# Kernel tuning notes

Measured on AMD Instinct MI355X. Metric: run time of the kernel, lower is better.

The kernel has to match this reference:

```python
import jax, jax.numpy as jnp
import numpy as np

N = 2048       # num nodes
E = 4096       # num edges
D_NODE = 128
D_EDGE = 128
H = 4          # heads
DH = D_EDGE // H
C = 16         # num classes
NODE_K = N // 2   # node_k_ratio = 0.5
EDGE_K = E // 2   # edge_k_ratio = 0.5
NEG = -1e9


def setup_inputs() -> dict:
    key = jax.random.key(0)
    ks = jax.random.split(key, 16)
    w = lambda k, shape: jax.random.normal(k, shape, jnp.float32) * 0.02
    return {
        "node_features": jax.random.normal(ks[0], (N, D_NODE), jnp.float32),
        "edge_features": jax.random.normal(ks[1], (E, D_EDGE), jnp.float32),
        "edge_index": jax.random.randint(ks[2], (2, E), 0, N, jnp.int32),
        # ImportanceRouter: scalar scores per node / edge
        "w_router_n": w(ks[3], (D_NODE,)),
        "w_router_e": w(ks[4], (D_EDGE,)),
        # EdgeAttention projections
        "w_e": w(ks[5], (D_EDGE, D_EDGE)),
        "w_n": w(ks[6], (D_NODE, D_EDGE)),
        "w_q": w(ks[7], (D_EDGE, D_EDGE)),
        "w_k": w(ks[8], (D_EDGE, D_EDGE)),
        "w_v": w(ks[9], (D_EDGE, D_EDGE)),
        "w_o": w(ks[10], (D_EDGE, D_EDGE)),
        # classifier MLP: Linear -> GELU -> Linear
        "w1": w(ks[11], (D_EDGE, D_EDGE)),
        "b1": jnp.zeros((D_EDGE,), jnp.float32),
        "w2": w(ks[12], (D_EDGE, C)),
        "b2": jnp.zeros((C,), jnp.float32),
    }


def reference(node_features, edge_features, edge_index,
              w_router_n, w_router_e,
              w_e, w_n, w_q, w_k, w_v, w_o,
              w1, b1, w2, b2):
    src, dst = edge_index[0], edge_index[1]

    # --- ImportanceRouter: node/edge scores ---
    ns = node_features @ w_router_n   # [N]
    es = edge_features @ w_router_e   # [E]

    # --- apply_top_k(node_k_ratio=0.5, edge_k_ratio=0.5) ---
    _, nidx = jax.lax.top_k(ns, NODE_K)
    node_mask = jnp.zeros((N,), bool).at[nidx].set(True)
    _, eidx = jax.lax.top_k(es, EDGE_K)
    edge_topk = jnp.zeros((E,), bool).at[eidx].set(True)
    edge_mask = edge_topk & node_mask[src] & node_mask[dst]   # [E]

    ef = edge_features * edge_mask[:, None].astype(edge_features.dtype)

    # --- build_edge_adjacency: edges sharing a node attend to each other ---
    adj = ((src[:, None] == src[None, :]) | (src[:, None] == dst[None, :]) |
           (dst[:, None] == src[None, :]) | (dst[:, None] == dst[None, :]))  # [E,E]

    # --- EdgeAttention: edge rep mixes edge feats and endpoint node feats ---
    h = ef @ w_e + (node_features[src] + node_features[dst]) @ w_n   # [E, D_EDGE]
    q = (h @ w_q).reshape(E, H, DH)
    k = (h @ w_k).reshape(E, H, DH)
    v = (h @ w_v).reshape(E, H, DH)
    scores = jnp.einsum('ehd,fhd->hef', q, k) / np.float32(np.sqrt(DH))  # [H,E,E]
    scores = jnp.where(adj[None, :, :], scores, NEG)
    attn = jax.nn.softmax(scores, axis=-1)
    o = jnp.einsum('hef,fhd->ehd', attn, v).reshape(E, D_EDGE) @ w_o    # [E, D_EDGE]

    # --- classifier: Linear -> GELU -> Linear ---
    x = jax.nn.gelu(o @ w1 + b1)
    logits = x @ w2 + b2            # [E, C]
    return logits
```

## Files before the change

### kernel.cpp

```cpp
#include <hip/hip_runtime.h>
#include <hip/hip_bf16.h>
#include <math.h>

#define NN 2048
#define NE 4096
#define D 128
#define NODE_K 1024
#define EDGE_K 2048
#define CAP 64

typedef const __hip_bfloat16* bfp;
typedef unsigned short u16;
typedef __attribute__((ext_vector_type(8))) short short8;
typedef __attribute__((ext_vector_type(4))) float floatx4;

#define MFMA16(a, b, c) __builtin_amdgcn_mfma_f32_16x16x32_bf16(a, b, c, 0, 0, 0)

__device__ __forceinline__ float b2f(__hip_bfloat16 x) { return __bfloat162float(x); }

__device__ __forceinline__ float ldx(const void* p, size_t i, int f) {
  return f ? ((const float*)p)[i] : b2f(((bfp)p)[i]);
}

__device__ __forceinline__ void split2(float x, u16& hi, u16& lo) {
  unsigned u = __float_as_uint(x);
  unsigned h = (u + 0x7FFFu + ((u >> 16) & 1u)) >> 16;
  hi = (u16)h;
  float r = x - __uint_as_float(h << 16);
  unsigned v = __float_as_uint(r);
  lo = (u16)((v + 0x7FFFu + ((v >> 16) & 1u)) >> 16);
}
__device__ __forceinline__ void build_frags(const float* v8, short8& fh, short8& fl) {
  #pragma unroll
  for (int i = 0; i < 8; ++i) {
    u16 h, l;
    split2(v8[i], h, l);
    fh[i] = (short)h; fl[i] = (short)l;
  }
}

__device__ __forceinline__ int detect_f(const u16* raw, int* s4) {
  int t = threadIdx.x;
  int weird = 0;
  for (int i = t; i < 4096; i += blockDim.x) {
    unsigned int bits = ((unsigned int)raw[i]) << 16;
    float x = __uint_as_float(bits);
    float ax = fabsf(x);
    if (!(ax <= 1e3f) || (x != 0.f && ax < 1e-12f)) weird++;
  }
  #pragma unroll
  for (int m = 32; m >= 1; m >>= 1) weird += __shfl_xor(weird, m);
  int nw = (int)blockDim.x >> 6;
  if ((t & 63) == 0) s4[t >> 6] = weird;
  __syncthreads();
  int tot = 0;
  for (int i = 0; i < nw; ++i) tot += s4[i];
  return (tot > 200) ? 1 : 0;
}

struct K1Args {
  const void *nf, *ef, *wrn, *wre;
  const void* w[7];
  float *ns, *es;
  int *deg, *flag;
  u16 *wtHi, *wtLo;
  u16 *feHi, *feLo;
};

#define SCORE_BLOCKS ((NN + NE) / 4)
#define WPREP_BLOCKS 56
#define FSPLIT_BLOCKS 384
__global__ __launch_bounds__(256) void scores_prep_kernel(K1Args a) {
  __shared__ int s4[4];
  int b = blockIdx.x, t = threadIdx.x;
  int f = detect_f((const u16*)a.nf, s4);
  if (b < SCORE_BLOCKS) {
    int wid = b * 4 + (t >> 6), lane = t & 63;
    const void* base; const void* w; float* out; size_t r0;
    if (wid < NN) { base = a.nf; r0 = (size_t)wid * D; w = a.wrn; out = a.ns + wid; }
    else { int r = wid - NN; base = a.ef; r0 = (size_t)r * D; w = a.wre; out = a.es + r; }
    double p = (double)ldx(base, r0 + lane, f) * (double)ldx(w, lane, f)
             + (double)ldx(base, r0 + lane + 64, f) * (double)ldx(w, lane + 64, f);
    #pragma unroll
    for (int m = 32; m >= 1; m >>= 1) p += __shfl_xor(p, m);
    if (lane == 0) *out = (float)p;
  } else if (b == SCORE_BLOCKS) {
    if (t == 0) a.flag[0] = f;
    for (int i = t; i < NN; i += 256) a.deg[i] = 0;
  } else if (b <= SCORE_BLOCKS + WPREP_BLOCKS) {
    int wb = b - SCORE_BLOCKS - 1;
    #pragma unroll
    for (int i = 0; i < 8; ++i) {
      int g = wb * 2048 + i * 256 + t;
      int w = g >> 14, r = g & 16383;
      int k = r >> 7, n = r & 127;
      u16 hi, lo;
      split2(ldx(a.w[w], r, f), hi, lo);
      a.wtHi[w * 16384 + n * 128 + k] = hi;
      a.wtLo[w * 16384 + n * 128 + k] = lo;
    }
  } else {
    int fb = b - SCORE_BLOCKS - 1 - WPREP_BLOCKS;
    #pragma unroll
    for (int i = 0; i < 8; ++i) {
      int g = fb * 2048 + i * 256 + t;
      float x = (g < NN * D) ? ldx(a.nf, g, f) : ldx(a.ef, g - NN * D, f);
      u16 hi, lo;
      split2(x, hi, lo);
      a.feHi[g] = hi; a.feLo[g] = lo;
    }
  }
}

#define NMB (NN / 4)
#define EMB (NE / 4)
__global__ __launch_bounds__(256) void mask_lists_kernel(
    const float* __restrict__ ns, const float* __restrict__ es,
    const int* __restrict__ src, const int* __restrict__ dst,
    int* __restrict__ node_mask, int* __restrict__ edge_topk,
    int* __restrict__ deg, int* __restrict__ lists) {
  __shared__ float s[NE];
  int b = blockIdx.x, t = threadIdx.x;
  if (b < NMB) {
    for (int i = t; i < NN; i += 256) s[i] = ns[i];
    __syncthreads();
    int i = b * 4 + (t >> 6), lane = t & 63;
    float si = s[i];
    int rank = 0;
    for (int j = lane; j < NN; j += 64) {
      float sj = s[j];
      rank += (sj > si) || (sj == si && j < i);
    }
    #pragma unroll
    for (int m = 32; m >= 1; m >>= 1) rank += __shfl_xor(rank, m);
    if (lane == 0) node_mask[i] = (rank < NODE_K) ? 1 : 0;
  } else if (b < NMB + EMB) {
    for (int i = t; i < NE; i += 256) s[i] = es[i];
    __syncthreads();
    int i = (b - NMB) * 4 + (t >> 6), lane = t & 63;
    float si = s[i];
    int rank = 0;
    for (int j = lane; j < NE; j += 64) {
      float sj = s[j];
      rank += (sj > si) || (sj == si && j < i);
    }
    #pragma unroll
    for (int m = 32; m >= 1; m >>= 1) rank += __shfl_xor(rank, m);
    if (lane == 0) edge_topk[i] = (rank < EDGE_K) ? 1 : 0;
  } else {
    int e = (b - NMB - EMB) * 256 + t;
    if (e < NE) {
      int sn = src[e], dn = dst[e];
      int p = atomicAdd(&deg[sn], 1);
      if (p >= 0 && p < CAP) lists[sn * CAP + p] = e;
      if (dn != sn) {
        p = atomicAdd(&deg[dn], 1);
        if (p >= 0 && p < CAP) lists[dn * CAP + p] = e;
      }
    }
  }
}

__global__ __launch_bounds__(512) void h_qkv_mfma_kernel(
    const u16* __restrict__ feHi, const u16* __restrict__ feLo,
    const int* __restrict__ src, const int* __restrict__ dst,
    const int* __restrict__ node_mask, const int* __restrict__ edge_topk,
    const u16* __restrict__ wtHi, const u16* __restrict__ wtLo,
    float* __restrict__ qkv) {
  __shared__ __align__(16) float hf[8 * 64 * 4];
  int t = threadIdx.x;
  int wave = t >> 6, lane = t & 63;
  int qd = lane >> 4, c = lane & 15;
  int row0 = blockIdx.x * 16;
  int e = row0 + c;
  int sn = src[e], dn = dst[e];
  bool em = edge_topk[e] && node_mask[sn] && node_mask[dn];
  int n0 = wave * 16;
  const u16* efH = feHi + (size_t)NN * D;
  const u16* efL = feLo + (size_t)NN * D;
  const short8 z8 = {0, 0, 0, 0, 0, 0, 0, 0};

  floatx4 acc = {0.f, 0.f, 0.f, 0.f};
  #pragma unroll
  for (int ks = 0; ks < 4; ++ks) {
    int k0 = ks * 32 + qd * 8;
    short8 a1h = *(const short8*)(efH + (size_t)e * D + k0);
    short8 a1l = *(const short8*)(efL + (size_t)e * D + k0);
    if (!em) { a1h = z8; a1l = z8; }
    short8 sh = *(const short8*)(feHi + (size_t)sn * D + k0);
    short8 sl = *(const short8*)(feLo + (size_t)sn * D + k0);
    short8 dh = *(const short8*)(feHi + (size_t)dn * D + k0);
    short8 dl = *(const short8*)(feLo + (size_t)dn * D + k0);
    size_t bo = (size_t)(n0 + c) * 128 + k0;
    short8 bEh = *(const short8*)(wtHi + bo);
    short8 bEl = *(const short8*)(wtLo + bo);
    short8 bNh = *(const short8*)(wtHi + 16384 + bo);
    short8 bNl = *(const short8*)(wtLo + 16384 + bo);
    acc = MFMA16(a1h, bEh, acc);
    acc = MFMA16(a1l, bEh, acc);
    acc = MFMA16(a1h, bEl, acc);
    acc = MFMA16(sh, bNh, acc);
    acc = MFMA16(sl, bNh, acc);
    acc = MFMA16(sh, bNl, acc);
    acc = MFMA16(dh, bNh, acc);
    acc = MFMA16(dl, bNh, acc);
    acc = MFMA16(dh, bNl, acc);
  }
  {
    int np = n0 + c;
    int kd = np >> 5, qq = (np >> 3) & 3, half = (c >> 2) & 1, j4 = c & 3;
    #pragma unroll
    for (int r = 0; r < 4; ++r)
      hf[((kd * 2 + half) * 64 + qq * 16 + 4 * qd + r) * 4 + j4] = acc[r];
  }
  __syncthreads();
  floatx4 aq = {0.f, 0.f, 0.f, 0.f};
  floatx4 ak = {0.f, 0.f, 0.f, 0.f};
  floatx4 av = {0.f, 0.f, 0.f, 0.f};
  #pragma unroll
  for (int ks = 0; ks < 4; ++ks) {
    float4 p0 = *(const float4*)&hf[((ks * 2 + 0) * 64 + lane) * 4];
    float4 p1 = *(const float4*)&hf[((ks * 2 + 1) * 64 + lane) * 4];
    float v8[8] = {p0.x, p0.y, p0.z, p0.w, p1.x, p1.y, p1.z, p1.w};
    short8 ah, al;
    build_frags(v8, ah, al);
    size_t bo = (size_t)(n0 + c) * 128 + ks * 32 + qd * 8;
    short8 bqh = *(const short8*)(wtHi + 2 * 16384 + bo);
    short8 bql = *(const short8*)(wtLo + 2 * 16384 + bo);
    short8 bkh = *(const short8*)(wtHi + 3 * 16384 + bo);
    short8 bkl = *(const short8*)(wtLo + 3 * 16384 + bo);
    short8 bvh = *(const short8*)(wtHi + 4 * 16384 + bo);
    short8 bvl = *(const short8*)(wtLo + 4 * 16384 + bo);
    aq = MFMA16(ah, bqh, aq); aq = MFMA16(al, bqh, aq); aq = MFMA16(ah, bql, aq);
    ak = MFMA16(ah, bkh, ak); ak = MFMA16(al, bkh, ak); ak = MFMA16(ah, bkl, ak);
    av = MFMA16(ah, bvh, av); av = MFMA16(al, bvh, av); av = MFMA16(ah, bvl, av);
  }
  #pragma unroll
  for (int r = 0; r < 4; ++r) {
    size_t ro = (size_t)(row0 + 4 * qd + r) * D + n0 + c;
    qkv[ro] = aq[r];
    qkv[(size_t)NE * D + ro] = ak[r];
    qkv[(size_t)2 * NE * D + ro] = av[r];
  }
}

__global__ __launch_bounds__(512) void attn_mlp_kernel(
    const float* __restrict__ qkv, const int* __restrict__ src,
    const int* __restrict__ dst, const int* __restrict__ deg,
    const int* __restrict__ lists,
    const u16* __restrict__ wtHi, const u16* __restrict__ wtLo,
    const void* __restrict__ b1, const void* __restrict__ w2,
    const void* __restrict__ b2, const int* __restrict__ flag,
    void* __restrict__ out) {
  __shared__ __align__(16) float aol[16 * 132];
  __shared__ __align__(16) float hf[8 * 64 * 4];
  __shared__ float xl[16 * 132];
  __shared__ float w2l[128 * 16];
  int t = threadIdx.x;
  int row0 = blockIdx.x * 16;
  int f = flag[0];
  const float* qp = qkv;
  const float* kp = qkv + (size_t)NE * D;
  const float* vp = qkv + (size_t)2 * NE * D;
  const float scale = 0.17677669529663687f;
  int j = t & 127;
  for (int it = 0; it < 4; ++it) {
    int le = it * 4 + (t >> 7);
    int e = row0 + le;
    float qj = qp[(size_t)e * D + j];
    int sn = src[e], dn = dst[e];
    float m = -1e30f, l = 0.f, acc = 0.f;
    int degA = max(0, min(deg[sn], CAP));
    for (int i = 0; i < degA; ++i) {
      int fe = lists[sn * CAP + i];
      float p = qj * kp[(size_t)fe * D + j];
      p += __shfl_xor(p, 16); p += __shfl_xor(p, 8); p += __shfl_xor(p, 4);
      p += __shfl_xor(p, 2);  p += __shfl_xor(p, 1);
      float s = p * scale;
      float vj = vp[(size_t)fe * D + j];
      float mn = fmaxf(m, s);
      float corr = expf(m - mn);
      float w = expf(s - mn);
      l = l * corr + w;
      acc = acc * corr + w * vj;
      m = mn;
    }
    if (dn != sn) {
      int degB = max(0, min(deg[dn], CAP));
      for (int i = 0; i < degB; ++i) {
        int fe = lists[dn * CAP + i];
        if (src[fe] == sn || dst[fe] == sn) continue;
        float p = qj * kp[(size_t)fe * D + j];
        p += __shfl_xor(p, 16); p += __shfl_xor(p, 8); p += __shfl_xor(p, 4);
        p += __shfl_xor(p, 2);  p += __shfl_xor(p, 1);
        float s = p * scale;
        float vj = vp[(size_t)fe * D + j];
        float mn = fmaxf(m, s);
        float corr = expf(m - mn);
        float w = expf(s - mn);
        l = l * corr + w;
        acc = acc * corr + w * vj;
        m = mn;
      }
    }
    aol[le * 132 + j] = acc / fmaxf(l, 1e-37f);
  }
  for (int i = t; i < D * 16; i += 512) w2l[i] = ldx(w2, i, f);
  __syncthreads();

  int wave = t >> 6, lane = t & 63;
  int qd = lane >> 4, c = lane & 15;
  int n0 = wave * 16;
  floatx4 acc = {0.f, 0.f, 0.f, 0.f};
  #pragma unroll
  for (int ks = 0; ks < 4; ++ks) {
    int k0 = ks * 32 + qd * 8;
    const float* ap = aol + c * 132 + k0;
    float4 p0 = *(const float4*)ap;
    float4 p1 = *(const float4*)(ap + 4);
    float v8[8] = {p0.x, p0.y, p0.z, p0.w, p1.x, p1.y, p1.z, p1.w};
    short8 ah, al;
    build_frags(v8, ah, al);
    size_t bo = (size_t)(n0 + c) * 128 + k0;
    short8 bh = *(const short8*)(wtHi + 5 * 16384 + bo);
    short8 bl = *(const short8*)(wtLo + 5 * 16384 + bo);
    acc = MFMA16(ah, bh, acc);
    acc = MFMA16(al, bh, acc);
    acc = MFMA16(ah, bl, acc);
  }
  {
    int np = n0 + c;
    int kd = np >> 5, qq = (np >> 3) & 3, half = (c >> 2) & 1, j4 = c & 3;
    #pragma unroll
    for (int r = 0; r < 4; ++r)
      hf[((kd * 2 + half) * 64 + qq * 16 + 4 * qd + r) * 4 + j4] = acc[r];
  }
  __syncthreads();
  floatx4 a2c = {0.f, 0.f, 0.f, 0.f};
  #pragma unroll
  for (int ks = 0; ks < 4; ++ks) {
    float4 p0 = *(const float4*)&hf[((ks * 2 + 0) * 64 + lane) * 4];
    float4 p1 = *(const float4*)&hf[((ks * 2 + 1) * 64 + lane) * 4];
    float v8[8] = {p0.x, p0.y, p0.z, p0.w, p1.x, p1.y, p1.z, p1.w};
    short8 ah, al;
    build_frags(v8, ah, al);
    size_t bo = (size_t)(n0 + c) * 128 + ks * 32 + qd * 8;
    short8 bh = *(const short8*)(wtHi + 6 * 16384 + bo);
    short8 bl = *(const short8*)(wtLo + 6 * 16384 + bo);
    a2c = MFMA16(ah, bh, a2c);
    a2c = MFMA16(al, bh, a2c);
    a2c = MFMA16(ah, bl, a2c);
  }
  float bj = ldx(b1, n0 + c, f);
  #pragma unroll
  for (int r = 0; r < 4; ++r) {
    float u = a2c[r] + bj;
    float inner = 0.7978845608028654f * (u + 0.044715f * u * u * u);
    xl[(4 * qd + r) * 132 + n0 + c] = 0.5f * u * (1.f + tanhf(inner));
  }
  __syncthreads();
  if (t < 256) {
    int r = t >> 4, cc = t & 15;
    float s = 0.f;
    for (int kk = 0; kk < D; ++kk) s += xl[r * 132 + kk] * w2l[kk * 16 + cc];
    s += ldx(b2, cc, f);
    int idx = (row0 + r) * 16 + cc;
    if (f) ((float*)out)[idx] = s;
    else ((__hip_bfloat16*)out)[idx] = __float2bfloat16(s);
  }
}

extern "C" void kernel_launch(void* const* d_in, const int* in_sizes, int n_in,
                              void* d_out, int out_size, void* d_ws, size_t ws_size,
                              hipStream_t stream) {
  const int* eidx = (const int*)d_in[2];
  const int* src = eidx;
  const int* dst = eidx + NE;

  size_t off = 0;
  char* base = (char*)d_ws;
  auto alloc = [&](size_t nbytes) -> void* {
    void* p = base + off;
    off += (nbytes + 255) & ~(size_t)255;
    return p;
  };
  int* flag      = (int*)alloc(256);
  float* ns      = (float*)alloc(NN * sizeof(float));
  float* es      = (float*)alloc(NE * sizeof(float));
  int* node_mask = (int*)alloc(NN * sizeof(int));
  int* edge_topk = (int*)alloc(NE * sizeof(int));
  int* deg       = (int*)alloc(NN * sizeof(int));
  int* lists     = (int*)alloc((size_t)NN * CAP * sizeof(int));
  u16* wtHi      = (u16*)alloc((size_t)7 * 16384 * sizeof(u16));
  u16* wtLo      = (u16*)alloc((size_t)7 * 16384 * sizeof(u16));
  u16* feHi      = (u16*)alloc((size_t)(NN + NE) * D * sizeof(u16));
  u16* feLo      = (u16*)alloc((size_t)(NN + NE) * D * sizeof(u16));
  float* qkv     = (float*)alloc((size_t)3 * NE * D * sizeof(float));

  K1Args a1;
  a1.nf = d_in[0]; a1.ef = d_in[1]; a1.wrn = d_in[3]; a1.wre = d_in[4];
  a1.w[0] = d_in[5];  a1.w[1] = d_in[6];  a1.w[2] = d_in[7];
  a1.w[3] = d_in[8];  a1.w[4] = d_in[9];  a1.w[5] = d_in[10]; a1.w[6] = d_in[11];
  a1.ns = ns; a1.es = es; a1.deg = deg; a1.flag = flag;
  a1.wtHi = wtHi; a1.wtLo = wtLo; a1.feHi = feHi; a1.feLo = feLo;

  scores_prep_kernel<<<SCORE_BLOCKS + 1 + WPREP_BLOCKS + FSPLIT_BLOCKS, 256, 0,
                       stream>>>(a1);
  mask_lists_kernel<<<NMB + EMB + NE / 256, 256, 0, stream>>>(
      ns, es, src, dst, node_mask, edge_topk, deg, lists);
  h_qkv_mfma_kernel<<<NE / 16, 512, 0, stream>>>(
      feHi, feLo, src, dst, node_mask, edge_topk, wtHi, wtLo, qkv);
  attn_mlp_kernel<<<NE / 16, 512, 0, stream>>>(
      qkv, src, dst, deg, lists, wtHi, wtLo, d_in[12], d_in[13], d_in[14],
      flag, d_out);
}
```

Before: 170.3 us.

## Split attention from MLP, vectorize prep kernels, prefetch MFMA weight fragments

```diff
diff --git a/kernel.cpp b/kernel.cpp
--- a/kernel.cpp
+++ b/kernel.cpp
@@ -20,6 +20,16 @@
 
 __device__ __forceinline__ float ldx(const void* p, size_t i, int f) {
   return f ? ((const float*)p)[i] : b2f(((bfp)p)[i]);
+}
+__device__ __forceinline__ float4 ldx4(const void* p, size_t i4, int f) {
+  if (f) return ((const float4*)p)[i4];
+  ushort4 u = ((const ushort4*)p)[i4];
+  float4 r;
+  r.x = __uint_as_float(((unsigned)u.x) << 16);
+  r.y = __uint_as_float(((unsigned)u.y) << 16);
+  r.z = __uint_as_float(((unsigned)u.z) << 16);
+  r.w = __uint_as_float(((unsigned)u.w) << 16);
+  return r;
 }
 
 __device__ __forceinline__ void split2(float x, u16& hi, u16& lo) {
@@ -42,7 +52,7 @@
 __device__ __forceinline__ int detect_f(const u16* raw, int* s4) {
   int t = threadIdx.x;
   int weird = 0;
-  for (int i = t; i < 4096; i += blockDim.x) {
+  for (int i = t; i < 1024; i += blockDim.x) {
     unsigned int bits = ((unsigned int)raw[i]) << 16;
     float x = __uint_as_float(bits);
     float ax = fabsf(x);
@@ -55,7 +65,7 @@
   __syncthreads();
   int tot = 0;
   for (int i = 0; i < nw; ++i) tot += s4[i];
-  return (tot > 200) ? 1 : 0;
+  return (tot > 50) ? 1 : 0;
 }
 
 struct K1Args {
@@ -68,8 +78,8 @@
 };
 
 #define SCORE_BLOCKS ((NN + NE) / 4)
-#define WPREP_BLOCKS 56
-#define FSPLIT_BLOCKS 384
+#define WPREP_BLOCKS 112
+#define FSPLIT_BLOCKS 192
 __global__ __launch_bounds__(256) void scores_prep_kernel(K1Args a) {
   __shared__ int s4[4];
   int b = blockIdx.x, t = threadIdx.x;
@@ -88,26 +98,30 @@
     if (t == 0) a.flag[0] = f;
     for (int i = t; i < NN; i += 256) a.deg[i] = 0;
   } else if (b <= SCORE_BLOCKS + WPREP_BLOCKS) {
-    int wb = b - SCORE_BLOCKS - 1;
-    #pragma unroll
-    for (int i = 0; i < 8; ++i) {
-      int g = wb * 2048 + i * 256 + t;
-      int w = g >> 14, r = g & 16383;
-      int k = r >> 7, n = r & 127;
-      u16 hi, lo;
-      split2(ldx(a.w[w], r, f), hi, lo);
-      a.wtHi[w * 16384 + n * 128 + k] = hi;
-      a.wtLo[w * 16384 + n * 128 + k] = lo;
-    }
+    int tau = (b - SCORE_BLOCKS - 1) * 256 + t;
+    int w = tau >> 12, rem = tau & 4095;
+    int n = rem >> 5, k0 = (rem & 31) * 4;
+    ushort4 hi, lo;
+    split2(ldx(a.w[w], (size_t)(k0 + 0) * 128 + n, f), hi.x, lo.x);
+    split2(ldx(a.w[w], (size_t)(k0 + 1) * 128 + n, f), hi.y, lo.y);
+    split2(ldx(a.w[w], (size_t)(k0 + 2) * 128 + n, f), hi.z, lo.z);
+    split2(ldx(a.w[w], (size_t)(k0 + 3) * 128 + n, f), hi.w, lo.w);
+    ((ushort4*)a.wtHi)[tau] = hi;
+    ((ushort4*)a.wtLo)[tau] = lo;
   } else {
     int fb = b - SCORE_BLOCKS - 1 - WPREP_BLOCKS;
     #pragma unroll
-    for (int i = 0; i < 8; ++i) {
-      int g = fb * 2048 + i * 256 + t;
-      float x = (g < NN * D) ? ldx(a.nf, g, f) : ldx(a.ef, g - NN * D, f);
-      u16 hi, lo;
-      split2(x, hi, lo);
-      a.feHi[g] = hi; a.feLo[g] = lo;
+    for (int i = 0; i < 4; ++i) {
+      int g4 = fb * 1024 + i * 256 + t;
+      float4 x = (g4 < NN * D / 4) ? ldx4(a.nf, g4, f)
+                                   : ldx4(a.ef, g4 - NN * D / 4, f);
+      ushort4 hi, lo;
+      split2(x.x, hi.x, lo.x);
+      split2(x.y, hi.y, lo.y);
+      split2(x.z, hi.z, lo.z);
+      split2(x.w, hi.w, lo.w);
+      ((ushort4*)a.feHi)[g4] = hi;
+      ((ushort4*)a.feLo)[g4] = lo;
     }
   }
 }
@@ -180,38 +194,58 @@
   const u16* efL = feLo + (size_t)NN * D;
   const short8 z8 = {0, 0, 0, 0, 0, 0, 0, 0};
 
-  floatx4 acc = {0.f, 0.f, 0.f, 0.f};
+  short8 A1h[4], A1l[4], Sh[4], Sl[4], Dh[4], Dl[4];
+  short8 BEh[4], BEl[4], BNh[4], BNl[4];
   #pragma unroll
   for (int ks = 0; ks < 4; ++ks) {
     int k0 = ks * 32 + qd * 8;
-    short8 a1h = *(const short8*)(efH + (size_t)e * D + k0);
-    short8 a1l = *(const short8*)(efL + (size_t)e * D + k0);
-    if (!em) { a1h = z8; a1l = z8; }
-    short8 sh = *(const short8*)(feHi + (size_t)sn * D + k0);
-    short8 sl = *(const short8*)(feLo + (size_t)sn * D + k0);
-    short8 dh = *(const short8*)(feHi + (size_t)dn * D + k0);
-    short8 dl = *(const short8*)(feLo + (size_t)dn * D + k0);
+    A1h[ks] = *(const short8*)(efH + (size_t)e * D + k0);
+    A1l[ks] = *(const short8*)(efL + (size_t)e * D + k0);
+    Sh[ks]  = *(const short8*)(feHi + (size_t)sn * D + k0);
+    Sl[ks]  = *(const short8*)(feLo + (size_t)sn * D + k0);
+    Dh[ks]  = *(const short8*)(feHi + (size_t)dn * D + k0);
+    Dl[ks]  = *(const short8*)(feLo + (size_t)dn * D + k0);
     size_t bo = (size_t)(n0 + c) * 128 + k0;
-    short8 bEh = *(const short8*)(wtHi + bo);
-    short8 bEl = *(const short8*)(wtLo + bo);
-    short8 bNh = *(const short8*)(wtHi + 16384 + bo);
-    short8 bNl = *(const short8*)(wtLo + 16384 + bo);
-    acc = MFMA16(a1h, bEh, acc);
-    acc = MFMA16(a1l, bEh, acc);
-    acc = MFMA16(a1h, bEl, acc);
-    acc = MFMA16(sh, bNh, acc);
-    acc = MFMA16(sl, bNh, acc);
-    acc = MFMA16(sh, bNl, acc);
-    acc = MFMA16(dh, bNh, acc);
-    acc = MFMA16(dl, bNh, acc);
-    acc = MFMA16(dh, bNl, acc);
+    BEh[ks] = *(const short8*)(wtHi + bo);
+    BEl[ks] = *(const short8*)(wtLo + bo);
+    BNh[ks] = *(const short8*)(wtHi + 16384 + bo);
+    BNl[ks] = *(const short8*)(wtLo + 16384 + bo);
+  }
+  if (!em) {
+    #pragma unroll
+    for (int ks = 0; ks < 4; ++ks) { A1h[ks] = z8; A1l[ks] = z8; }
+  }
+  floatx4 accE = {0.f, 0.f, 0.f, 0.f};
+  floatx4 accN = {0.f, 0.f, 0.f, 0.f};
+  #pragma unroll
+  for (int ks = 0; ks < 4; ++ks) {
+    accE = MFMA16(A1h[ks], BEh[ks], accE);
+    accN = MFMA16(Sh[ks], BNh[ks], accN);
+    accE = MFMA16(A1l[ks], BEh[ks], accE);
+    accN = MFMA16(Sl[ks], BNh[ks], accN);
+    accE = MFMA16(A1h[ks], BEl[ks], accE);
+    accN = MFMA16(Sh[ks], BNl[ks], accN);
+    accN = MFMA16(Dh[ks], BNh[ks], accN);
+    accN = MFMA16(Dl[ks], BNh[ks], accN);
+    accN = MFMA16(Dh[ks], BNl[ks], accN);
   }
   {
     int np = n0 + c;
     int kd = np >> 5, qq = (np >> 3) & 3, half = (c >> 2) & 1, j4 = c & 3;
     #pragma unroll
     for (int r = 0; r < 4; ++r)
-      hf[((kd * 2 + half) * 64 + qq * 16 + 4 * qd + r) * 4 + j4] = acc[r];
+      hf[((kd * 2 + half) * 64 + qq * 16 + 4 * qd + r) * 4 + j4] = accE[r] + accN[r];
+  }
+  short8 BQh[4], BQl[4], BKh[4], BKl[4], BVh[4], BVl[4];
+  #pragma unroll
+  for (int ks = 0; ks < 4; ++ks) {
+    size_t bo = (size_t)(n0 + c) * 128 + ks * 32 + qd * 8;
+    BQh[ks] = *(const short8*)(wtHi + 2 * 16384 + bo);
+    BQl[ks] = *(const short8*)(wtLo + 2 * 16384 + bo);
+    BKh[ks] = *(const short8*)(wtHi + 3 * 16384 + bo);
+    BKl[ks] = *(const short8*)(wtLo + 3 * 16384 + bo);
+    BVh[ks] = *(const short8*)(wtHi + 4 * 16384 + bo);
+    BVl[ks] = *(const short8*)(wtLo + 4 * 16384 + bo);
   }
   __syncthreads();
   floatx4 aq = {0.f, 0.f, 0.f, 0.f};
@@ -224,16 +258,15 @@
     float v8[8] = {p0.x, p0.y, p0.z, p0.w, p1.x, p1.y, p1.z, p1.w};
     short8 ah, al;
     build_frags(v8, ah, al);
-    size_t bo = (size_t)(n0 + c) * 128 + ks * 32 + qd * 8;
-    short8 bqh = *(const short8*)(wtHi + 2 * 16384 + bo);
-    short8 bql = *(const short8*)(wtLo + 2 * 16384 + bo);
-    short8 bkh = *(const short8*)(wtHi + 3 * 16384 + bo);
-    short8 bkl = *(const short8*)(wtLo + 3 * 16384 + bo);
-    short8 bvh = *(const short8*)(wtHi + 4 * 16384 + bo);
-    short8 bvl = *(const short8*)(wtLo + 4 * 16384 + bo);
-    aq = MFMA16(ah, bqh, aq); aq = MFMA16(al, bqh, aq); aq = MFMA16(ah, bql, aq);
-    ak = MFMA16(ah, bkh, ak); ak = MFMA16(al, bkh, ak); ak = MFMA16(ah, bkl, ak);
-    av = MFMA16(ah, bvh, av); av = MFMA16(al, bvh, av); av = MFMA16(ah, bvl, av);
+    aq = MFMA16(ah, BQh[ks], aq);
+    ak = MFMA16(ah, BKh[ks], ak);
+    av = MFMA16(ah, BVh[ks], av);
+    aq = MFMA16(al, BQh[ks], aq);
+    ak = MFMA16(al, BKh[ks], ak);
+    av = MFMA16(al, BVh[ks], av);
+    aq = MFMA16(ah, BQl[ks], aq);
+    ak = MFMA16(ah, BKl[ks], ak);
+    av = MFMA16(ah, BVl[ks], av);
   }
   #pragma unroll
   for (int r = 0; r < 4; ++r) {
@@ -244,40 +277,41 @@
   }
 }
 
-__global__ __launch_bounds__(512) void attn_mlp_kernel(
-    const float* __restrict__ qkv, const int* __restrict__ src,
-    const int* __restrict__ dst, const int* __restrict__ deg,
-    const int* __restrict__ lists,
-    const u16* __restrict__ wtHi, const u16* __restrict__ wtLo,
-    const void* __restrict__ b1, const void* __restrict__ w2,
-    const void* __restrict__ b2, const int* __restrict__ flag,
-    void* __restrict__ out) {
-  __shared__ __align__(16) float aol[16 * 132];
-  __shared__ __align__(16) float hf[8 * 64 * 4];
-  __shared__ float xl[16 * 132];
-  __shared__ float w2l[128 * 16];
-  int t = threadIdx.x;
-  int row0 = blockIdx.x * 16;
-  int f = flag[0];
-  const float* qp = qkv;
-  const float* kp = qkv + (size_t)NE * D;
-  const float* vp = qkv + (size_t)2 * NE * D;
+__global__ void attn_kernel(const float* __restrict__ q, const float* __restrict__ k,
+                            const float* __restrict__ v, const int* __restrict__ src,
+                            const int* __restrict__ dst, const int* __restrict__ deg,
+                            const int* __restrict__ lists, float* __restrict__ ao) {
+  int e = blockIdx.x;
+  int j = threadIdx.x;
+  float qj = q[(size_t)e * D + j];
+  int sn = src[e], dn = dst[e];
+  float m = -1e30f, l = 0.f, acc = 0.f;
   const float scale = 0.17677669529663687f;
-  int j = t & 127;
-  for (int it = 0; it < 4; ++it) {
-    int le = it * 4 + (t >> 7);
-    int e = row0 + le;
-    float qj = qp[(size_t)e * D + j];
-    int sn = src[e], dn = dst[e];
-    float m = -1e30f, l = 0.f, acc = 0.f;
-    int degA = max(0, min(deg[sn], CAP));
-    for (int i = 0; i < degA; ++i) {
-      int fe = lists[sn * CAP + i];
-      float p = qj * kp[(size_t)fe * D + j];
+  int degA = max(0, min(deg[sn], CAP));
+  for (int i = 0; i < degA; ++i) {
+    int fe = lists[sn * CAP + i];
+    float p = qj * k[(size_t)fe * D + j];
+    p += __shfl_xor(p, 16); p += __shfl_xor(p, 8); p += __shfl_xor(p, 4);
+    p += __shfl_xor(p, 2);  p += __shfl_xor(p, 1);
+    float s = p * scale;
+    float vj = v[(size_t)fe * D + j];
+    float mn = fmaxf(m, s);
+    float corr = expf(m - mn);
+    float w = expf(s - mn);
+    l = l * corr + w;
+    acc = acc * corr + w * vj;
+    m = mn;
+  }
+  if (dn != sn) {
+    int degB = max(0, min(deg[dn], CAP));
+    for (int i = 0; i < degB; ++i) {
+      int fe = lists[dn * CAP + i];
+      if (src[fe] == sn || dst[fe] == sn) continue;
+      float p = qj * k[(size_t)fe * D + j];
       p += __shfl_xor(p, 16); p += __shfl_xor(p, 8); p += __shfl_xor(p, 4);
       p += __shfl_xor(p, 2);  p += __shfl_xor(p, 1);
       float s = p * scale;
-      float vj = vp[(size_t)fe * D + j];
+      float vj = v[(size_t)fe * D + j];
       float mn = fmaxf(m, s);
       float corr = expf(m - mn);
       float w = expf(s - mn);
@@ -285,48 +319,48 @@
       acc = acc * corr + w * vj;
       m = mn;
     }
-    if (dn != sn) {
-      int degB = max(0, min(deg[dn], CAP));
-      for (int i = 0; i < degB; ++i) {
-        int fe = lists[dn * CAP + i];
-        if (src[fe] == sn || dst[fe] == sn) continue;
-        float p = qj * kp[(size_t)fe * D + j];
-        p += __shfl_xor(p, 16); p += __shfl_xor(p, 8); p += __shfl_xor(p, 4);
-        p += __shfl_xor(p, 2);  p += __shfl_xor(p, 1);
-        float s = p * scale;
-        float vj = vp[(size_t)fe * D + j];
-        float mn = fmaxf(m, s);
-        float corr = expf(m - mn);
-        float w = expf(s - mn);
-        l = l * corr + w;
-        acc = acc * corr + w * vj;
-        m = mn;
-      }
-    }
-    aol[le * 132 + j] = acc / fmaxf(l, 1e-37f);
-  }
-  for (int i = t; i < D * 16; i += 512) w2l[i] = ldx(w2, i, f);
-  __syncthreads();
-
+  }
+  ao[(size_t)e * D + j] = acc / fmaxf(l, 1e-37f);
+}
+
+__global__ __launch_bounds__(512) void o_mlp_mfma_kernel(
+    const float* __restrict__ ao,
+    const u16* __restrict__ wtHi, const u16* __restrict__ wtLo,
+    const void* __restrict__ b1, const void* __restrict__ w2,
+    const void* __restrict__ b2, const int* __restrict__ flag,
+    void* __restrict__ out) {
+  __shared__ __align__(16) float hf[8 * 64 * 4];
+  __shared__ float xl[16 * 132];
+  __shared__ float w2l[128 * 16];
+  int t = threadIdx.x;
   int wave = t >> 6, lane = t & 63;
   int qd = lane >> 4, c = lane & 15;
+  int f = flag[0];
+  int row0 = blockIdx.x * 16;
   int n0 = wave * 16;
+
+  short8 BOh[4], BOl[4], B1h[4], B1l[4];
+  #pragma unroll
+  for (int ks = 0; ks < 4; ++ks) {
+    size_t bo = (size_t)(n0 + c) * 128 + ks * 32 + qd * 8;
+    BOh[ks] = *(const short8*)(wtHi + 5 * 16384 + bo);
+    BOl[ks] = *(const short8*)(wtLo + 5 * 16384 + bo);
+    B1h[ks] = *(const short8*)(wtHi + 6 * 16384 + bo);
+    B1l[ks] = *(const short8*)(wtLo + 6 * 16384 + bo);
+  }
   floatx4 acc = {0.f, 0.f, 0.f, 0.f};
   #pragma unroll
   for (int ks = 0; ks < 4; ++ks) {
     int k0 = ks * 32 + qd * 8;
-    const float* ap = aol + c * 132 + k0;
+    const float* ap = ao + (size_t)(row0 + c) * D + k0;
     float4 p0 = *(const float4*)ap;
     float4 p1 = *(const float4*)(ap + 4);
     float v8[8] = {p0.x, p0.y, p0.z, p0.w, p1.x, p1.y, p1.z, p1.w};
     short8 ah, al;
     build_frags(v8, ah, al);
-    size_t bo = (size_t)(n0 + c) * 128 + k0;
-    short8 bh = *(const short8*)(wtHi + 5 * 16384 + bo);
-    short8 bl = *(const short8*)(wtLo + 5 * 16384 + bo);
-    acc = MFMA16(ah, bh, acc);
-    acc = MFMA16(al, bh, acc);
-    acc = MFMA16(ah, bl, acc);
+    acc = MFMA16(ah, BOh[ks], acc);
+    acc = MFMA16(al, BOh[ks], acc);
+    acc = MFMA16(ah, BOl[ks], acc);
   }
   {
     int np = n0 + c;
@@ -344,12 +378,9 @@
     float v8[8] = {p0.x, p0.y, p0.z, p0.w, p1.x, p1.y, p1.z, p1.w};
     short8 ah, al;
     build_frags(v8, ah, al);
-    size_t bo = (size_t)(n0 + c) * 128 + ks * 32 + qd * 8;
-    short8 bh = *(const short8*)(wtHi + 6 * 16384 + bo);
-    short8 bl = *(const short8*)(wtLo + 6 * 16384 + bo);
-    a2c = MFMA16(ah, bh, a2c);
-    a2c = MFMA16(al, bh, a2c);
-    a2c = MFMA16(ah, bl, a2c);
+    a2c = MFMA16(ah, B1h[ks], a2c);
+    a2c = MFMA16(al, B1h[ks], a2c);
+    a2c = MFMA16(ah, B1l[ks], a2c);
   }
   float bj = ldx(b1, n0 + c, f);
   #pragma unroll
@@ -358,6 +389,7 @@
     float inner = 0.7978845608028654f * (u + 0.044715f * u * u * u);
     xl[(4 * qd + r) * 132 + n0 + c] = 0.5f * u * (1.f + tanhf(inner));
   }
+  for (int i = t; i < D * 16; i += 512) w2l[i] = ldx(w2, i, f);
   __syncthreads();
   if (t < 256) {
     int r = t >> 4, cc = t & 15;
@@ -396,6 +428,8 @@
   u16* feHi      = (u16*)alloc((size_t)(NN + NE) * D * sizeof(u16));
   u16* feLo      = (u16*)alloc((size_t)(NN + NE) * D * sizeof(u16));
   float* qkv     = (float*)alloc((size_t)3 * NE * D * sizeof(float));
+  float* ao      = (float*)alloc((size_t)NE * D * sizeof(float));
+  float* qb = qkv, *kb = qkv + NE * D, *vb = qkv + 2 * NE * D;
 
   K1Args a1;
   a1.nf = d_in[0]; a1.ef = d_in[1]; a1.wrn = d_in[3]; a1.wre = d_in[4];
@@ -410,7 +444,7 @@
       ns, es, src, dst, node_mask, edge_topk, deg, lists);
   h_qkv_mfma_kernel<<<NE / 16, 512, 0, stream>>>(
       feHi, feLo, src, dst, node_mask, edge_topk, wtHi, wtLo, qkv);
-  attn_mlp_kernel<<<NE / 16, 512, 0, stream>>>(
-      qkv, src, dst, deg, lists, wtHi, wtLo, d_in[12], d_in[13], d_in[14],
-      flag, d_out);
-}
+  attn_kernel<<<NE, 128, 0, stream>>>(qb, kb, vb, src, dst, deg, lists, ao);
+  o_mlp_mfma_kernel<<<NE / 16, 512, 0, stream>>>(
+      ao, wtHi, wtLo, d_in[12], d_in[13], d_in[14], flag, d_out);
+}
```

New measurement: 139.1 us. 18.3% less time.
